# Kernel tuning notes

Hardware: AMD Instinct MI355X
Metric: run time of the kernel (lower is better)

The kernel has to match this reference:

```python
import jax, jax.numpy as jnp
import numpy as np

NUM_HEADS = 8
NUM_CHUNKS, INPUT_DIM = 50000, 768
HIDDEN_DIM, OUTPUT_DIM = 512, 256
NUM_CELLS, MAX_LEN = 2048, 64


def setup_inputs() -> dict:
    key = jax.random.key(0)
    ks = jax.random.split(key, 16)
    s = 0.02
    return {
        "chunk_features": jax.random.normal(ks[0], (NUM_CHUNKS, INPUT_DIM), jnp.float32),
        # q/k/v input projections (nn.Linear: y = x @ W.T + b)
        "Wq": jax.random.normal(ks[1], (HIDDEN_DIM, INPUT_DIM), jnp.float32) * s,
        "bq": jnp.zeros((HIDDEN_DIM,), jnp.float32),
        "Wk": jax.random.normal(ks[2], (HIDDEN_DIM, INPUT_DIM), jnp.float32) * s,
        "bk": jnp.zeros((HIDDEN_DIM,), jnp.float32),
        "Wv": jax.random.normal(ks[3], (HIDDEN_DIM, INPUT_DIM), jnp.float32) * s,
        "bv": jnp.zeros((HIDDEN_DIM,), jnp.float32),
        # nn.MultiheadAttention internal in_proj (stacked q,k,v) and out_proj
        "W_in": jax.random.normal(ks[4], (3 * HIDDEN_DIM, HIDDEN_DIM), jnp.float32) * s,
        "b_in": jnp.zeros((3 * HIDDEN_DIM,), jnp.float32),
        "Wo": jax.random.normal(ks[5], (HIDDEN_DIM, HIDDEN_DIM), jnp.float32) * s,
        "bo": jnp.zeros((HIDDEN_DIM,), jnp.float32),
        # final output projection
        "Wout": jax.random.normal(ks[6], (OUTPUT_DIM, HIDDEN_DIM), jnp.float32) * s,
        "bout": jnp.zeros((OUTPUT_DIM,), jnp.float32),
        # ragged cells packed as padded indices + lengths
        "cell_idx": jax.random.randint(ks[7], (NUM_CELLS, MAX_LEN), 0, NUM_CHUNKS, jnp.int64),
        "cell_len": jax.random.randint(ks[8], (NUM_CELLS,), 0, MAX_LEN, jnp.int64),
    }


def reference(chunk_features, Wq, bq, Wk, bk, Wv, bv, W_in, b_in, Wo, bo,
              Wout, bout, cell_idx, cell_len):
    C, L = cell_idx.shape
    H = Wq.shape[0]
    hd = H // NUM_HEADS
    dt = chunk_features.dtype
    lengths = jnp.maximum(cell_len, 1)                       # at least 1 valid chunk per cell
    mask = jnp.arange(L)[None, :] < lengths[:, None]         # [C, L] valid-position mask

    x = chunk_features[cell_idx]                             # [C, L, D] ragged gather (padded)
    q = x @ Wq.T + bq                                        # [C, L, H]
    k = x @ Wk.T + bk
    v = x @ Wv.T + bv

    # MultiheadAttention's own in_proj on top of q/k/v
    Wiq, Wik, Wiv = jnp.split(W_in, 3, axis=0)
    biq, bik, biv = jnp.split(b_in, 3)
    qi = (q @ Wiq.T + biq).reshape(C, L, NUM_HEADS, hd)
    ki = (k @ Wik.T + bik).reshape(C, L, NUM_HEADS, hd)
    vi = (v @ Wiv.T + biv).reshape(C, L, NUM_HEADS, hd)

    scale = jnp.asarray(1.0 / np.sqrt(hd), dt)
    scores = jnp.einsum('clhd,cmhd->chlm', qi, ki) * scale   # [C, nH, L, L]
    scores = jnp.where(mask[:, None, None, :], scores, jnp.asarray(-1e30, dt))
    attn = jax.nn.softmax(scores, axis=-1)
    ctx = jnp.einsum('chlm,cmhd->clhd', attn, vi).reshape(C, L, H)
    out = ctx @ Wo.T + bo                                    # MHA out_proj

    # masked mean-pool over valid chunk positions, then final projection
    pooled = (out * mask[..., None]).sum(axis=1) / lengths[:, None].astype(dt)
    return pooled @ Wout.T + bout                            # [C, OUTPUT_DIM]
```

## Files before the change

kernel.cpp:

```cpp
#include <hip/hip_runtime.h>

typedef short s16x8 __attribute__((ext_vector_type(8)));
typedef float f32x4 __attribute__((ext_vector_type(4)));
typedef unsigned short u16;

static __device__ __forceinline__ f32x4 mfma16(s16x8 a, s16x8 b, f32x4 c) {
  return __builtin_amdgcn_mfma_f32_16x16x32_bf16(a, b, c, 0, 0, 0);
}

static __device__ __forceinline__ u16 f2b(float f) {
  union { float f; unsigned int u; } v; v.f = f;
  unsigned int u = v.u;
  return (u16)((u + 0x7fffu + ((u >> 16) & 1u)) >> 16);
}
static __device__ __forceinline__ float b2f(u16 h) {
  union { float f; unsigned int u; } v; v.u = ((unsigned int)h) << 16;
  return v.f;
}

static __device__ __forceinline__ void gld_lds16(const void* g, void* l) {
  __builtin_amdgcn_global_load_lds(
      (const __attribute__((address_space(1))) void*)g,
      (__attribute__((address_space(3))) void*)l, 16, 0, 0);
}

template<int MODE>
static __device__ void gemm_tile(const float* __restrict__ A,
                                 const float* __restrict__ B,
                                 void* __restrict__ Cout,
                                 int m0, int n0, int K, int lda, int ldb, int ldc,
                                 u16 (*As)[40], u16 (*BsT)[40]) {
  const int tid = threadIdx.x;
  const int wave = tid >> 6, lane = tid & 63;
  const int quad = lane >> 4, l16 = lane & 15;
  f32x4 acc[4] = {{0,0,0,0},{0,0,0,0},{0,0,0,0},{0,0,0,0}};
  for (int k0 = 0; k0 < K; k0 += 32) {
    __syncthreads();
    {
      const int r = tid >> 2, cs = (tid & 3) << 3;
      const float* ap = A + (size_t)(m0 + r) * lda + k0 + cs;
      float4 v0 = *(const float4*)ap, v1 = *(const float4*)(ap + 4);
      As[r][cs+0] = f2b(v0.x); As[r][cs+1] = f2b(v0.y);
      As[r][cs+2] = f2b(v0.z); As[r][cs+3] = f2b(v0.w);
      As[r][cs+4] = f2b(v1.x); As[r][cs+5] = f2b(v1.y);
      As[r][cs+6] = f2b(v1.z); As[r][cs+7] = f2b(v1.w);
    }
    {
      const int kk = tid >> 3, ns = (tid & 7) << 3;
      const float* bp = B + (size_t)(k0 + kk) * ldb + n0 + ns;
      float4 v0 = *(const float4*)bp, v1 = *(const float4*)(bp + 4);
      BsT[ns+0][kk] = f2b(v0.x); BsT[ns+1][kk] = f2b(v0.y);
      BsT[ns+2][kk] = f2b(v0.z); BsT[ns+3][kk] = f2b(v0.w);
      BsT[ns+4][kk] = f2b(v1.x); BsT[ns+5][kk] = f2b(v1.y);
      BsT[ns+6][kk] = f2b(v1.z); BsT[ns+7][kk] = f2b(v1.w);
    }
    __syncthreads();
    const s16x8 af = *(const s16x8*)&As[(wave << 4) + l16][quad << 3];
    #pragma unroll
    for (int nt = 0; nt < 4; nt++) {
      const s16x8 bfr = *(const s16x8*)&BsT[(nt << 4) + l16][quad << 3];
      acc[nt] = mfma16(af, bfr, acc[nt]);
    }
  }
  const int mrow = m0 + (wave << 4) + (quad << 2);
  #pragma unroll
  for (int nt = 0; nt < 4; nt++) {
    const int n = n0 + (nt << 4) + l16;
    #pragma unroll
    for (int r = 0; r < 4; r++) {
      const float v = acc[nt][r];
      if (MODE == 0) ((u16*)Cout)[(size_t)(mrow + r) * ldc + n] = f2b(v);
      else           ((float*)Cout)[(size_t)(mrow + r) * ldc + n] = v;
    }
  }
}

__global__ __launch_bounds__(256)
void prep_all(const float* __restrict__ chunk,
              const float* __restrict__ Wq, const float* __restrict__ bq,
              const float* __restrict__ Wk, const float* __restrict__ bk,
              const float* __restrict__ Wv, const float* __restrict__ bv,
              const float* __restrict__ W_in, const float* __restrict__ b_in,
              const float* __restrict__ Wo, const float* __restrict__ bo,
              const float* __restrict__ Wout, const float* __restrict__ bout,
              u16* __restrict__ Wqkv, float* __restrict__ Wv_eff,
              float* __restrict__ Wf, float* __restrict__ b_eff,
              float* __restrict__ b2, u16* __restrict__ Xb) {
  __shared__ u16 As[64][40];
  __shared__ u16 BsT[64][40];
  __shared__ float t1s[512];
  __shared__ float t2s[512];
  const int b = blockIdx.x;
  const int tid = threadIdx.x;

  if (b < 96) {
    gemm_tile<0>(W_in, Wq, Wqkv, (b / 12) << 6, (b % 12) << 6, 512, 512, 768, 768, As, BsT);
  } else if (b < 192) {
    const int bb = b - 96;
    gemm_tile<0>(W_in + 512 * 512, Wk, Wqkv + 512 * 768,
                 (bb / 12) << 6, (bb % 12) << 6, 512, 512, 768, 768, As, BsT);
  } else if (b < 288) {
    const int bb = b - 192;
    gemm_tile<3>(W_in + 1024 * 512, Wv, Wv_eff,
                 (bb / 12) << 6, (bb % 12) << 6, 512, 512, 768, 768, As, BsT);
  } else if (b < 320) {
    const int bb = b - 288;
    gemm_tile<3>(Wout, Wo, Wf, (bb / 8) << 6, (bb % 8) << 6, 512, 512, 512, 512, As, BsT);
  } else if (b == 320) {
    for (int j = tid; j < 512; j += 256) {
      const float* ar = W_in + (size_t)(1024 + j) * 512;
      float acc = 0.f;
      for (int k = 0; k < 512; k += 4) {
        float4 w = *(const float4*)(ar + k);
        acc += w.x * bv[k] + w.y * bv[k+1] + w.z * bv[k+2] + w.w * bv[k+3];
      }
      t1s[j] = acc + b_in[1024 + j];
    }
    __syncthreads();
    for (int j = tid; j < 512; j += 256) {
      const float* ar = Wo + (size_t)j * 512;
      float acc = 0.f;
      for (int k = 0; k < 512; k += 4) {
        float4 w = *(const float4*)(ar + k);
        acc += w.x * t1s[k] + w.y * t1s[k+1] + w.z * t1s[k+2] + w.w * t1s[k+3];
      }
      t2s[j] = acc + bo[j];
    }
    __syncthreads();
    if (tid < 256) {
      const float* ar = Wout + (size_t)tid * 512;
      float acc = 0.f;
      for (int k = 0; k < 512; k += 4) {
        float4 w = *(const float4*)(ar + k);
        acc += w.x * t2s[k] + w.y * t2s[k+1] + w.z * t2s[k+2] + w.w * t2s[k+3];
      }
      b2[tid] = acc + bout[tid];
    }
    for (int j = tid; j < 512; j += 256) {
      const float* aq = W_in + (size_t)j * 512;
      const float* ak = W_in + (size_t)(512 + j) * 512;
      float accq = 0.f, acck = 0.f;
      for (int k = 0; k < 512; k += 4) {
        float4 wq4 = *(const float4*)(aq + k);
        float4 wk4 = *(const float4*)(ak + k);
        accq += wq4.x * bq[k] + wq4.y * bq[k+1] + wq4.z * bq[k+2] + wq4.w * bq[k+3];
        acck += wk4.x * bk[k] + wk4.y * bk[k+1] + wk4.z * bk[k+2] + wk4.w * bk[k+3];
      }
      b_eff[j] = accq + b_in[j];
      b_eff[512 + j] = acck + b_in[512 + j];
    }
  } else {
    const size_t i = (((size_t)(b - 321)) * 256 + tid) << 3;
    ushort4 lo, hi;
    if (i < (size_t)50000 * 768) {
      const float4 a = *(const float4*)(chunk + i);
      const float4 bb = *(const float4*)(chunk + i + 4);
      lo.x = f2b(a.x); lo.y = f2b(a.y); lo.z = f2b(a.z); lo.w = f2b(a.w);
      hi.x = f2b(bb.x); hi.y = f2b(bb.y); hi.z = f2b(bb.z); hi.w = f2b(bb.w);
    } else {
      lo.x = lo.y = lo.z = lo.w = 0; hi.x = hi.y = hi.z = hi.w = 0;
    }
    *(ushort4*)(Xb + i) = lo;
    *(ushort4*)(Xb + i + 4) = hi;
  }
}

__global__ __launch_bounds__(256)
void qk_mh(const u16* __restrict__ Xb, const u16* __restrict__ W,
           const float* __restrict__ bias, u16* __restrict__ QK2,
           const float* __restrict__ Wf, const float* __restrict__ Wv_eff,
           u16* __restrict__ Mh) {
  __shared__ char smem[16384];
  const int gb = blockIdx.x;
  const int tid = threadIdx.x;

  if (gb >= 3128) {
    const int bb = gb - 3128;
    const int z = bb / 48, r = bb % 48;
    u16 (*As40)[40] = (u16(*)[40])smem;
    u16 (*Bs40)[40] = (u16(*)[40])(smem + 5120);
    gemm_tile<0>(Wf + z * 64, Wv_eff + (size_t)z * 64 * 768, Mh + z * 768,
                 (r / 12) << 6, (r % 12) << 6, 64, 512, 768, 6144, As40, Bs40);
    return;
  }

  u16* As = (u16*)smem;
  u16* Bs = (u16*)(smem + 8192);
  const int xcd = gb & 7;
  const int lin = xcd * 391 + (gb >> 3);
  const int n0 = (lin & 7) << 7;
  const int m0 = (lin >> 3) << 7;
  const int wave = tid >> 6, lane = tid & 63;
  const int wm = wave >> 1, wn = wave & 1;
  const int quad = lane >> 4, l16 = lane & 15;

  const int r0 = (wave << 5) + (lane >> 2);
  const int cb = (lane & 3) << 3;
  const u16* gA = Xb + (size_t)(m0 + r0) * 768 + cb;
  const u16* gB = W  + (size_t)(n0 + r0) * 768 + cb;
  u16* lA = As + (wave << 10);
  u16* lB = Bs + (wave << 10);

  f32x4 acc[4][4];
  #pragma unroll
  for (int i = 0; i < 4; i++)
    #pragma unroll
    for (int j = 0; j < 4; j++) acc[i][j] = (f32x4){0.f, 0.f, 0.f, 0.f};

  for (int k0 = 0; k0 < 768; k0 += 32) {
    __syncthreads();
    gld_lds16(gA + k0,            lA);
    gld_lds16(gA + k0 + 16 * 768, lA + 512);
    gld_lds16(gB + k0,            lB);
    gld_lds16(gB + k0 + 16 * 768, lB + 512);
    __syncthreads();
    s16x8 af[4], bf[4];
    #pragma unroll
    for (int i = 0; i < 4; i++)
      af[i] = *(const s16x8*)(As + ((wm << 6) + (i << 4) + l16) * 32 + (quad << 3));
    #pragma unroll
    for (int j = 0; j < 4; j++)
      bf[j] = *(const s16x8*)(Bs + ((wn << 6) + (j << 4) + l16) * 32 + (quad << 3));
    #pragma unroll
    for (int i = 0; i < 4; i++)
      #pragma unroll
      for (int j = 0; j < 4; j++)
        acc[i][j] = mfma16(af[i], bf[j], acc[i][j]);
  }

  #pragma unroll
  for (int j = 0; j < 4; j++) {
    const int col = n0 + (wn << 6) + (j << 4) + l16;
    const float badd = bias[col];
    #pragma unroll
    for (int i = 0; i < 4; i++) {
      const int row = m0 + (wm << 6) + (i << 4) + (quad << 2);
      #pragma unroll
      for (int r = 0; r < 4; r++)
        QK2[(size_t)(row + r) * 1024 + col] = f2b(acc[i][j][r] + badd);
    }
  }
}

__global__ __launch_bounds__(256)
void attn_pool(const u16* __restrict__ QK2, const u16* __restrict__ Xb,
               const int* __restrict__ cell_idx, const int* __restrict__ cell_len,
               u16* __restrict__ Xbar) {
  __shared__ int idx_s[64];
  __shared__ float Sf[64][66];
  __shared__ float wl[512];

  const int c = blockIdx.x;
  const int tid = threadIdx.x;
  const int wave = tid >> 6, lane = tid & 63;
  const int quad = lane >> 4, l16 = lane & 15;

  int len = cell_len[c];
  len = (len < 1) ? 1 : ((len > 64) ? 64 : len);
  const int mt = (len + 15) >> 4;
  const float invLen = 1.0f / (float)len;

  if (tid < 64) idx_s[tid] = cell_idx[(c << 6) + tid];
  __syncthreads();

  for (int h = 0; h < 8; h++) {
    for (int item = wave; item < mt * mt; item += 4) {
      const int mq = item / mt, mk = item - mq * mt;
      const size_t qrow = (size_t)idx_s[(mq << 4) + l16] * 1024;
      const size_t krow = (size_t)idx_s[(mk << 4) + l16] * 1024;
      f32x4 s = {0.f, 0.f, 0.f, 0.f};
      #pragma unroll
      for (int ks = 0; ks < 2; ks++) {
        const s16x8 a = *(const s16x8*)(QK2 + qrow + (h << 6) + (ks << 5) + (quad << 3));
        const s16x8 b = *(const s16x8*)(QK2 + krow + 512 + (h << 6) + (ks << 5) + (quad << 3));
        s = mfma16(a, b, s);
      }
      const int col = (mk << 4) + l16, rb = (mq << 4) + (quad << 2);
      Sf[rb+0][col] = s[0]; Sf[rb+1][col] = s[1];
      Sf[rb+2][col] = s[2]; Sf[rb+3][col] = s[3];
    }
    __syncthreads();

    {
      const int row = tid >> 2, sub = tid & 3, c0 = sub << 4;
      if (row < len) {
        float ev[16];
        float mx = -3e38f;
        #pragma unroll
        for (int t = 0; t < 16; t++) {
          const int cc = c0 + t;
          const float v = (cc < len) ? Sf[row][cc] : -3e38f;
          ev[t] = v; mx = fmaxf(mx, v);
        }
        mx = fmaxf(mx, __shfl_xor(mx, 1));
        mx = fmaxf(mx, __shfl_xor(mx, 2));
        float sum = 0.f;
        #pragma unroll
        for (int t = 0; t < 16; t++) {
          const int cc = c0 + t;
          const float e = (cc < len) ? __expf((ev[t] - mx) * 0.125f) : 0.f;
          ev[t] = e; sum += e;
        }
        sum += __shfl_xor(sum, 1);
        sum += __shfl_xor(sum, 2);
        const float inv = 1.0f / sum;
        #pragma unroll
        for (int t = 0; t < 16; t++) Sf[row][c0 + t] = ev[t] * inv;
      }
    }
    __syncthreads();

    if (tid < 64) {
      float s = 0.f;
      if (tid < len)
        for (int l = 0; l < len; l++) s += Sf[l][tid];
      wl[(h << 6) + tid] = s * invLen;
    }
    __syncthreads();
  }

  if (tid < 192) {
    const int d0 = tid << 2;
    float acc[8][4];
    #pragma unroll
    for (int h = 0; h < 8; h++)
      #pragma unroll
      for (int d = 0; d < 4; d++) acc[h][d] = 0.f;
    for (int m = 0; m < len; m++) {
      const ushort4 xv = *(const ushort4*)(Xb + (size_t)idx_s[m] * 768 + d0);
      const float x0 = b2f(xv.x), x1 = b2f(xv.y), x2 = b2f(xv.z), x3 = b2f(xv.w);
      #pragma unroll
      for (int h = 0; h < 8; h++) {
        const float wv = wl[(h << 6) + m];
        acc[h][0] += wv * x0; acc[h][1] += wv * x1;
        acc[h][2] += wv * x2; acc[h][3] += wv * x3;
      }
    }
    #pragma unroll
    for (int h = 0; h < 8; h++) {
      ushort4 o;
      o.x = f2b(acc[h][0]); o.y = f2b(acc[h][1]);
      o.z = f2b(acc[h][2]); o.w = f2b(acc[h][3]);
      *(ushort4*)(Xbar + (size_t)c * 6144 + (h * 768) + d0) = o;
    }
  }
}

__global__ __launch_bounds__(256)
void gemm_final(const u16* __restrict__ A, const u16* __restrict__ B,
                const float* __restrict__ bias, float* __restrict__ out) {
  __shared__ u16 As[64 * 32];
  __shared__ u16 Bs[64 * 32];
  const int tid = threadIdx.x;
  const int wave = tid >> 6, lane = tid & 63;
  const int quad = lane >> 4, l16 = lane & 15;
  const int m0 = blockIdx.y << 6, n0 = blockIdx.x << 6;

  const int r = lane >> 2, c8 = (lane & 3) << 3;
  const u16* gA = A + (size_t)(m0 + (wave << 4) + r) * 6144 + c8;
  const u16* gB = B + (size_t)(n0 + (wave << 4) + r) * 6144 + c8;
  u16* lA = As + (wave << 9);
  u16* lB = Bs + (wave << 9);

  f32x4 acc[4] = {{0,0,0,0},{0,0,0,0},{0,0,0,0},{0,0,0,0}};
  for (int k0 = 0; k0 < 6144; k0 += 32) {
    __syncthreads();
    gld_lds16(gA + k0, lA);
    gld_lds16(gB + k0, lB);
    __syncthreads();
    const s16x8 a = *(const s16x8*)(As + ((wave << 4) + l16) * 32 + (quad << 3));
    #pragma unroll
    for (int j = 0; j < 4; j++) {
      const s16x8 b = *(const s16x8*)(Bs + ((j << 4) + l16) * 32 + (quad << 3));
      acc[j] = mfma16(a, b, acc[j]);
    }
  }
  const int row = m0 + (wave << 4) + (quad << 2);
  #pragma unroll
  for (int j = 0; j < 4; j++) {
    const int col = n0 + (j << 4) + l16;
    const float badd = bias[col];
    #pragma unroll
    for (int r2 = 0; r2 < 4; r2++)
      out[(size_t)(row + r2) * 256 + col] = acc[j][r2] + badd;
  }
}

extern "C" void kernel_launch(void* const* d_in, const int* in_sizes, int n_in,
                              void* d_out, int out_size, void* d_ws, size_t ws_size,
                              hipStream_t stream) {
  const float* chunk  = (const float*)d_in[0];
  const float* Wq     = (const float*)d_in[1];
  const float* bq     = (const float*)d_in[2];
  const float* Wk     = (const float*)d_in[3];
  const float* bk     = (const float*)d_in[4];
  const float* Wv     = (const float*)d_in[5];
  const float* bv     = (const float*)d_in[6];
  const float* W_in   = (const float*)d_in[7];
  const float* b_in   = (const float*)d_in[8];
  const float* Wo     = (const float*)d_in[9];
  const float* bo     = (const float*)d_in[10];
  const float* Wout   = (const float*)d_in[11];
  const float* bout   = (const float*)d_in[12];
  const int* cell_idx = (const int*)d_in[13];
  const int* cell_len = (const int*)d_in[14];

  char* ws = (char*)d_ws;
  u16*   Wqkv   = (u16*)(ws + 0);
  float* Wv_eff = (float*)(ws + 1572864);
  float* Wf     = (float*)(ws + 3145728);
  float* b_eff  = (float*)(ws + 3670016);
  float* b2     = (float*)(ws + 3674112);
  u16*   Mh     = (u16*)(ws + 3675136);
  u16*   Xbar   = (u16*)(ws + 6820864);
  u16*   Xb     = (u16*)(ws + 31986688);
  u16*   QK2    = (u16*)(ws + 108860416);

  dim3 blk(256);
  prep_all<<<dim3(19089), blk, 0, stream>>>(chunk, Wq, bq, Wk, bk, Wv, bv,
      W_in, b_in, Wo, bo, Wout, bout, Wqkv, Wv_eff, Wf, b_eff, b2, Xb);
  qk_mh<<<dim3(3512), blk, 0, stream>>>(Xb, Wqkv, b_eff, QK2, Wf, Wv_eff, Mh);
  attn_pool<<<dim3(2048), blk, 0, stream>>>(QK2, Xb, cell_idx, cell_len, Xbar);
  gemm_final<<<dim3(4, 32), blk, 0, stream>>>(Xbar, Mh, b2, (float*)d_out);
}
```

Baseline: 659.7 us.

## Register-resident per-wave attention, split-K final GEMM, grid-stride bf16 conversion

The attention stage now gives each wave two heads and computes the score tiles, the masked softmax and the column sums entirely in registers using cross-lane shuffles. This removes the shared-memory score matrix and the per-head block barriers. The final GEMM is split along K into 6 partial slabs, followed by a small reduction kernel that adds the bias, so many more blocks run than the previous 128. The chunk-to-bf16 conversion uses a grid-stride loop with far fewer blocks. In exchange it adds an extra launch, writes and reads the partial buffers, and uses more registers for the larger tiles.

```diff
diff --git a/kernel.cpp b/kernel.cpp
--- a/kernel.cpp
+++ b/kernel.cpp
@@ -150,18 +150,21 @@
       b_eff[512 + j] = acck + b_in[512 + j];
     }
   } else {
-    const size_t i = (((size_t)(b - 321)) * 256 + tid) << 3;
-    ushort4 lo, hi;
-    if (i < (size_t)50000 * 768) {
-      const float4 a = *(const float4*)(chunk + i);
-      const float4 bb = *(const float4*)(chunk + i + 4);
-      lo.x = f2b(a.x); lo.y = f2b(a.y); lo.z = f2b(a.z); lo.w = f2b(a.w);
-      hi.x = f2b(bb.x); hi.y = f2b(bb.y); hi.z = f2b(bb.z); hi.w = f2b(bb.w);
-    } else {
-      lo.x = lo.y = lo.z = lo.w = 0; hi.x = hi.y = hi.z = hi.w = 0;
-    }
-    *(ushort4*)(Xb + i) = lo;
-    *(ushort4*)(Xb + i + 4) = hi;
+    const size_t stride = 2048 * 256;
+    for (size_t g = (size_t)(b - 321) * 256 + tid; g < 4804608ull; g += stride) {
+      const size_t i = g << 3;
+      ushort4 lo, hi;
+      if (i < (size_t)50000 * 768) {
+        const float4 a = *(const float4*)(chunk + i);
+        const float4 bb = *(const float4*)(chunk + i + 4);
+        lo.x = f2b(a.x); lo.y = f2b(a.y); lo.z = f2b(a.z); lo.w = f2b(a.w);
+        hi.x = f2b(bb.x); hi.y = f2b(bb.y); hi.z = f2b(bb.z); hi.w = f2b(bb.w);
+      } else {
+        lo.x = lo.y = lo.z = lo.w = 0; hi.x = hi.y = hi.z = hi.w = 0;
+      }
+      *(ushort4*)(Xb + i) = lo;
+      *(ushort4*)(Xb + i + 4) = hi;
+    }
   }
 }
 
@@ -242,12 +245,90 @@
   }
 }
 
+template<int MT>
+static __device__ __forceinline__ void head_sw(
+    const u16* __restrict__ QK2, const int* __restrict__ idx_s,
+    float* __restrict__ wl, const int h, const int len, const float invLen,
+    const int quad, const int l16) {
+  f32x4 sacc[MT][MT];
+  #pragma unroll
+  for (int mq = 0; mq < MT; mq++)
+    #pragma unroll
+    for (int mk = 0; mk < MT; mk++) sacc[mq][mk] = (f32x4){0.f, 0.f, 0.f, 0.f};
+
+  #pragma unroll
+  for (int ks = 0; ks < 2; ks++) {
+    s16x8 qa[MT], kb[MT];
+    #pragma unroll
+    for (int mq = 0; mq < MT; mq++)
+      qa[mq] = *(const s16x8*)(QK2 + (size_t)idx_s[(mq << 4) + l16] * 1024
+                               + (h << 6) + (ks << 5) + (quad << 3));
+    #pragma unroll
+    for (int mk = 0; mk < MT; mk++)
+      kb[mk] = *(const s16x8*)(QK2 + (size_t)idx_s[(mk << 4) + l16] * 1024 + 512
+                               + (h << 6) + (ks << 5) + (quad << 3));
+    #pragma unroll
+    for (int mq = 0; mq < MT; mq++)
+      #pragma unroll
+      for (int mk = 0; mk < MT; mk++)
+        sacc[mq][mk] = mfma16(qa[mq], kb[mk], sacc[mq][mk]);
+  }
+
+  #pragma unroll
+  for (int mk = 0; mk < MT; mk++) {
+    if (((mk << 4) + l16) >= len) {
+      #pragma unroll
+      for (int mq = 0; mq < MT; mq++)
+        sacc[mq][mk] = (f32x4){-3e38f, -3e38f, -3e38f, -3e38f};
+    }
+  }
+
+  #pragma unroll
+  for (int mq = 0; mq < MT; mq++) {
+    #pragma unroll
+    for (int r = 0; r < 4; r++) {
+      float mx = sacc[mq][0][r];
+      #pragma unroll
+      for (int mk = 1; mk < MT; mk++) mx = fmaxf(mx, sacc[mq][mk][r]);
+      mx = fmaxf(mx, __shfl_xor(mx, 1));
+      mx = fmaxf(mx, __shfl_xor(mx, 2));
+      mx = fmaxf(mx, __shfl_xor(mx, 4));
+      mx = fmaxf(mx, __shfl_xor(mx, 8));
+      float sum = 0.f;
+      #pragma unroll
+      for (int mk = 0; mk < MT; mk++) {
+        const float e = __expf((sacc[mq][mk][r] - mx) * 0.125f);
+        sacc[mq][mk][r] = e; sum += e;
+      }
+      sum += __shfl_xor(sum, 1);
+      sum += __shfl_xor(sum, 2);
+      sum += __shfl_xor(sum, 4);
+      sum += __shfl_xor(sum, 8);
+      const float inv = 1.0f / sum;
+      #pragma unroll
+      for (int mk = 0; mk < MT; mk++) sacc[mq][mk][r] *= inv;
+    }
+  }
+
+  #pragma unroll
+  for (int mk = 0; mk < MT; mk++) {
+    float cs = 0.f;
+    #pragma unroll
+    for (int mq = 0; mq < MT; mq++)
+      #pragma unroll
+      for (int r = 0; r < 4; r++)
+        cs += (((mq << 4) + (quad << 2) + r) < len) ? sacc[mq][mk][r] : 0.f;
+    cs += __shfl_xor(cs, 16);
+    cs += __shfl_xor(cs, 32);
+    if (quad == 0) wl[(h << 6) + (mk << 4) + l16] = cs * invLen;
+  }
+}
+
 __global__ __launch_bounds__(256)
 void attn_pool(const u16* __restrict__ QK2, const u16* __restrict__ Xb,
                const int* __restrict__ cell_idx, const int* __restrict__ cell_len,
                u16* __restrict__ Xbar) {
   __shared__ int idx_s[64];
-  __shared__ float Sf[64][66];
   __shared__ float wl[512];
 
   const int c = blockIdx.x;
@@ -263,61 +344,26 @@
   if (tid < 64) idx_s[tid] = cell_idx[(c << 6) + tid];
   __syncthreads();
 
-  for (int h = 0; h < 8; h++) {
-    for (int item = wave; item < mt * mt; item += 4) {
-      const int mq = item / mt, mk = item - mq * mt;
-      const size_t qrow = (size_t)idx_s[(mq << 4) + l16] * 1024;
-      const size_t krow = (size_t)idx_s[(mk << 4) + l16] * 1024;
-      f32x4 s = {0.f, 0.f, 0.f, 0.f};
-      #pragma unroll
-      for (int ks = 0; ks < 2; ks++) {
-        const s16x8 a = *(const s16x8*)(QK2 + qrow + (h << 6) + (ks << 5) + (quad << 3));
-        const s16x8 b = *(const s16x8*)(QK2 + krow + 512 + (h << 6) + (ks << 5) + (quad << 3));
-        s = mfma16(a, b, s);
-      }
-      const int col = (mk << 4) + l16, rb = (mq << 4) + (quad << 2);
-      Sf[rb+0][col] = s[0]; Sf[rb+1][col] = s[1];
-      Sf[rb+2][col] = s[2]; Sf[rb+3][col] = s[3];
-    }
-    __syncthreads();
-
-    {
-      const int row = tid >> 2, sub = tid & 3, c0 = sub << 4;
-      if (row < len) {
-        float ev[16];
-        float mx = -3e38f;
-        #pragma unroll
-        for (int t = 0; t < 16; t++) {
-          const int cc = c0 + t;
-          const float v = (cc < len) ? Sf[row][cc] : -3e38f;
-          ev[t] = v; mx = fmaxf(mx, v);
-        }
-        mx = fmaxf(mx, __shfl_xor(mx, 1));
-        mx = fmaxf(mx, __shfl_xor(mx, 2));
-        float sum = 0.f;
-        #pragma unroll
-        for (int t = 0; t < 16; t++) {
-          const int cc = c0 + t;
-          const float e = (cc < len) ? __expf((ev[t] - mx) * 0.125f) : 0.f;
-          ev[t] = e; sum += e;
-        }
-        sum += __shfl_xor(sum, 1);
-        sum += __shfl_xor(sum, 2);
-        const float inv = 1.0f / sum;
-        #pragma unroll
-        for (int t = 0; t < 16; t++) Sf[row][c0 + t] = ev[t] * inv;
-      }
-    }
-    __syncthreads();
-
-    if (tid < 64) {
-      float s = 0.f;
-      if (tid < len)
-        for (int l = 0; l < len; l++) s += Sf[l][tid];
-      wl[(h << 6) + tid] = s * invLen;
-    }
-    __syncthreads();
-  }
+  const int h0 = wave << 1;
+  switch (mt) {
+    case 1:
+      head_sw<1>(QK2, idx_s, wl, h0,     len, invLen, quad, l16);
+      head_sw<1>(QK2, idx_s, wl, h0 + 1, len, invLen, quad, l16);
+      break;
+    case 2:
+      head_sw<2>(QK2, idx_s, wl, h0,     len, invLen, quad, l16);
+      head_sw<2>(QK2, idx_s, wl, h0 + 1, len, invLen, quad, l16);
+      break;
+    case 3:
+      head_sw<3>(QK2, idx_s, wl, h0,     len, invLen, quad, l16);
+      head_sw<3>(QK2, idx_s, wl, h0 + 1, len, invLen, quad, l16);
+      break;
+    default:
+      head_sw<4>(QK2, idx_s, wl, h0,     len, invLen, quad, l16);
+      head_sw<4>(QK2, idx_s, wl, h0 + 1, len, invLen, quad, l16);
+      break;
+  }
+  __syncthreads();
 
   if (tid < 192) {
     const int d0 = tid << 2;
@@ -347,23 +393,24 @@
 }
 
 __global__ __launch_bounds__(256)
-void gemm_final(const u16* __restrict__ A, const u16* __restrict__ B,
-                const float* __restrict__ bias, float* __restrict__ out) {
+void gemm_final_ks(const u16* __restrict__ A, const u16* __restrict__ B,
+                   float* __restrict__ partial) {
   __shared__ u16 As[64 * 32];
   __shared__ u16 Bs[64 * 32];
   const int tid = threadIdx.x;
   const int wave = tid >> 6, lane = tid & 63;
   const int quad = lane >> 4, l16 = lane & 15;
   const int m0 = blockIdx.y << 6, n0 = blockIdx.x << 6;
+  const int z = blockIdx.z;
 
   const int r = lane >> 2, c8 = (lane & 3) << 3;
-  const u16* gA = A + (size_t)(m0 + (wave << 4) + r) * 6144 + c8;
-  const u16* gB = B + (size_t)(n0 + (wave << 4) + r) * 6144 + c8;
+  const u16* gA = A + (size_t)(m0 + (wave << 4) + r) * 6144 + (z << 10) + c8;
+  const u16* gB = B + (size_t)(n0 + (wave << 4) + r) * 6144 + (z << 10) + c8;
   u16* lA = As + (wave << 9);
   u16* lB = Bs + (wave << 9);
 
   f32x4 acc[4] = {{0,0,0,0},{0,0,0,0},{0,0,0,0},{0,0,0,0}};
-  for (int k0 = 0; k0 < 6144; k0 += 32) {
+  for (int k0 = 0; k0 < 1024; k0 += 32) {
     __syncthreads();
     gld_lds16(gA + k0, lA);
     gld_lds16(gB + k0, lB);
@@ -375,15 +422,31 @@
       acc[j] = mfma16(a, b, acc[j]);
     }
   }
+  float* pz = partial + (size_t)z * 524288;
   const int row = m0 + (wave << 4) + (quad << 2);
   #pragma unroll
   for (int j = 0; j < 4; j++) {
     const int col = n0 + (j << 4) + l16;
-    const float badd = bias[col];
     #pragma unroll
     for (int r2 = 0; r2 < 4; r2++)
-      out[(size_t)(row + r2) * 256 + col] = acc[j][r2] + badd;
-  }
+      pz[(size_t)(row + r2) * 256 + col] = acc[j][r2];
+  }
+}
+
+__global__ __launch_bounds__(256)
+void reduce_out(const float* __restrict__ partial, const float* __restrict__ b2,
+                float* __restrict__ out) {
+  const size_t base = ((size_t)blockIdx.x * 256 + threadIdx.x) << 2;
+  float4 s = *(const float4*)(partial + base);
+  #pragma unroll
+  for (int z = 1; z < 6; z++) {
+    const float4 p = *(const float4*)(partial + (size_t)z * 524288 + base);
+    s.x += p.x; s.y += p.y; s.z += p.z; s.w += p.w;
+  }
+  const int col = (int)(base & 255);
+  const float4 bb = *(const float4*)(b2 + col);
+  s.x += bb.x; s.y += bb.y; s.z += bb.z; s.w += bb.w;
+  *(float4*)(out + base) = s;
 }
 
 extern "C" void kernel_launch(void* const* d_in, const int* in_sizes, int n_in,
@@ -406,20 +469,22 @@
   const int* cell_len = (const int*)d_in[14];
 
   char* ws = (char*)d_ws;
-  u16*   Wqkv   = (u16*)(ws + 0);
-  float* Wv_eff = (float*)(ws + 1572864);
-  float* Wf     = (float*)(ws + 3145728);
-  float* b_eff  = (float*)(ws + 3670016);
-  float* b2     = (float*)(ws + 3674112);
-  u16*   Mh     = (u16*)(ws + 3675136);
-  u16*   Xbar   = (u16*)(ws + 6820864);
-  u16*   Xb     = (u16*)(ws + 31986688);
-  u16*   QK2    = (u16*)(ws + 108860416);
+  u16*   Wqkv    = (u16*)(ws + 0);
+  float* Wv_eff  = (float*)(ws + 1572864);
+  float* Wf      = (float*)(ws + 3145728);
+  float* b_eff   = (float*)(ws + 3670016);
+  float* b2      = (float*)(ws + 3674112);
+  u16*   Mh      = (u16*)(ws + 3675136);
+  u16*   Xbar    = (u16*)(ws + 6820864);
+  u16*   Xb      = (u16*)(ws + 31986688);
+  u16*   QK2     = (u16*)(ws + 108860416);
+  float* partial = (float*)(ws + 211358720);
 
   dim3 blk(256);
-  prep_all<<<dim3(19089), blk, 0, stream>>>(chunk, Wq, bq, Wk, bk, Wv, bv,
+  prep_all<<<dim3(2369), blk, 0, stream>>>(chunk, Wq, bq, Wk, bk, Wv, bv,
       W_in, b_in, Wo, bo, Wout, bout, Wqkv, Wv_eff, Wf, b_eff, b2, Xb);
   qk_mh<<<dim3(3512), blk, 0, stream>>>(Xb, Wqkv, b_eff, QK2, Wf, Wv_eff, Mh);
   attn_pool<<<dim3(2048), blk, 0, stream>>>(QK2, Xb, cell_idx, cell_len, Xbar);
-  gemm_final<<<dim3(4, 32), blk, 0, stream>>>(Xbar, Mh, b2, (float*)d_out);
-}
+  gemm_final_ks<<<dim3(4, 32, 6), blk, 0, stream>>>(Xbar, Mh, partial);
+  reduce_out<<<dim3(512), blk, 0, stream>>>(partial, b2, (float*)d_out);
+}
```

Result: faster. 596.1 us (-9.6%).
